# Kernel tuning notes

Measured on AMD Instinct MI355X. Metric: run time of the kernel, lower is better.

## Reference

```python
import jax, jax.numpy as jnp
import numpy as np

E = 8        # n_experts
K = 2        # top_k
D = 1024     # n_embed
H = 2048     # moe_n_hidden
B, T = 4, 2048


def setup_inputs() -> dict:
    key = jax.random.key(0)
    ks = jax.random.split(key, 6)
    s = 0.02
    return {
        "x": jax.random.normal(ks[0], (B, T, D), dtype=jnp.float32),
        "Wr": jax.random.normal(ks[1], (D, E), dtype=jnp.float32) * s,   # router weight
        "W1": jax.random.normal(ks[2], (E, D, 2 * H), dtype=jnp.float32) * s,
        "b1": jnp.zeros((E, 2 * H), dtype=jnp.float32),
        "W2": jax.random.normal(ks[3], (E, H, D), dtype=jnp.float32) * s,
        "b2": jnp.zeros((E, D), dtype=jnp.float32),
    }


def reference(x, Wr, W1, b1, W2, b2):
    b, t, d = x.shape
    # router logits (noise=0, temp=1.0)
    z = jnp.einsum('btd,de->bte', x, Wr)                 # [B,T,E]
    vals, idx = jax.lax.top_k(z, K)                      # [B,T,K]
    gates = jax.nn.softmax(vals, axis=-1)                # [B,T,K]
    # combine weights per (token, expert): sum_k gate_k * 1[idx_k == e]
    onehot = jax.nn.one_hot(idx, E, dtype=x.dtype)       # [B,T,K,E]
    comb = jnp.einsum('btk,btke->bte', gates, onehot).reshape(b * t, E)
    xf = x.reshape(b * t, d)                             # [N,D]
    out = jnp.zeros_like(xf)
    for e in range(E):  # fixed small loop over structurally-distinct experts
        ab = xf @ W1[e] + b1[e]                          # [N,2H]
        a, bb = jnp.split(ab, 2, axis=-1)
        h = jax.nn.silu(a) * bb                          # swiGLU
        y = h @ W2[e] + b2[e]                            # [N,D]
        out = out + comb[:, e:e + 1] * y
    return out.reshape(b, t, d)
```

## Files before the change

### kernel.cpp

```cpp
#include <hip/hip_runtime.h>


#define N_TOK 8192
#define DIM   1024
#define HID   2048
#define NEXP  8
#define NK    (N_TOK * 2)
#define MAXT2 72
#define MAXT1 136

typedef __attribute__((ext_vector_type(8))) short short8;
typedef __attribute__((ext_vector_type(4))) float f32x4;

#define BARX() __builtin_amdgcn_s_barrier()
#define FEN()  asm volatile("" ::: "memory")
#define VMW2() asm volatile("s_waitcnt vmcnt(2)" ::: "memory")
#define VMW1() asm volatile("s_waitcnt vmcnt(1)" ::: "memory")
#define VMW0() asm volatile("s_waitcnt vmcnt(0)" ::: "memory")
#define PRIO(p) __builtin_amdgcn_s_setprio(p)

static __device__ __forceinline__ unsigned short f2bf(float f) {
  unsigned int u = __float_as_uint(f);
  u += 0x7fffu + ((u >> 16) & 1u);
  return (unsigned short)(u >> 16);
}

static __device__ __forceinline__ void glds16(const void* g, void* l) {
  __builtin_amdgcn_global_load_lds(
      (const __attribute__((address_space(1))) unsigned int*)g,
      (__attribute__((address_space(3))) unsigned int*)l, 16, 0, 0);
}

__device__ __forceinline__ void transpose_tile(const float* __restrict__ s,
                                               unsigned short* __restrict__ d,
                                               int R, int C, int c0, int r0,
                                               unsigned short (*tT)[68]) {
  int tid = threadIdx.x;
  int c = tid & 63, rq = tid >> 6;
#pragma unroll
  for (int q = 0; q < 4; ++q) {
    int rb = q * 16 + rq * 4;
    ushort4 v;
    v.x = f2bf(s[(size_t)(r0 + rb + 0) * C + c0 + c]);
    v.y = f2bf(s[(size_t)(r0 + rb + 1) * C + c0 + c]);
    v.z = f2bf(s[(size_t)(r0 + rb + 2) * C + c0 + c]);
    v.w = f2bf(s[(size_t)(r0 + rb + 3) * C + c0 + c]);
    *(ushort4*)&tT[c][rb] = v;
  }
  __syncthreads();
#pragma unroll
  for (int it = 0; it < 4; ++it) {
    int idx = it * 256 + tid;
    int cc = idx >> 4;
    int r4 = (idx & 15) * 4;
    *(ushort4*)(d + (size_t)(c0 + cc) * R + r0 + r4) = *(const ushort4*)&tT[cc][r4];
  }
}

__global__ __launch_bounds__(256) void prep_k(
    const float* __restrict__ x, const float* __restrict__ Wr,
    const float* __restrict__ W1, const float* __restrict__ W2,
    unsigned short* __restrict__ w1t, unsigned short* __restrict__ w2t,
    unsigned short* __restrict__ xb, int* __restrict__ te,
    float* __restrict__ tg, float* __restrict__ out) {
  __shared__ unsigned short tT[64][68];
  int bid = blockIdx.x;
  if (bid < 8192) {
    int z = bid >> 10, rem = bid & 1023;
    int c0 = (rem & 63) * 64, r0 = (rem >> 6) * 64;
    transpose_tile(W1 + (size_t)z * DIM * 2 * HID,
                   w1t + (size_t)z * DIM * 2 * HID, DIM, 2 * HID, c0, r0, tT);
  } else if (bid < 12288) {
    int b2 = bid - 8192;
    int z = b2 >> 9, rem = b2 & 511;
    int c0 = (rem & 15) * 64, r0 = (rem >> 4) * 64;
    transpose_tile(W2 + (size_t)z * HID * DIM,
                   w2t + (size_t)z * HID * DIM, HID, DIM, c0, r0, tT);
  } else if (bid < 14336) {
    int n = (bid - 12288) * 4 + (threadIdx.x >> 6);
    int lane = threadIdx.x & 63;
    float z[8];
#pragma unroll
    for (int e = 0; e < 8; ++e) z[e] = 0.f;
    const float* xr = x + (size_t)n * DIM;
    unsigned short* xbr = xb + (size_t)n * DIM;
#pragma unroll 4
    for (int i = 0; i < DIM / 64; ++i) {
      int d = lane + i * 64;
      float xv = xr[d];
      xbr[d] = f2bf(xv);
      float4 w0 = *(const float4*)(Wr + (size_t)d * 8);
      float4 w1 = *(const float4*)(Wr + (size_t)d * 8 + 4);
      z[0] += xv * w0.x; z[1] += xv * w0.y; z[2] += xv * w0.z; z[3] += xv * w0.w;
      z[4] += xv * w1.x; z[5] += xv * w1.y; z[6] += xv * w1.z; z[7] += xv * w1.w;
    }
    for (int off = 32; off; off >>= 1)
#pragma unroll
      for (int e = 0; e < 8; ++e) z[e] += __shfl_down(z[e], off);
    if (lane == 0) {
      int e0 = 0; float v0 = z[0];
#pragma unroll
      for (int e = 1; e < 8; ++e) if (z[e] > v0) { v0 = z[e]; e0 = e; }
      int e1 = -1; float v1 = -3.4e38f;
#pragma unroll
      for (int e = 0; e < 8; ++e) if (e != e0 && z[e] > v1) { v1 = z[e]; e1 = e; }
      float r = expf(v1 - v0);
      float s0 = 1.f / (1.f + r);
      te[n * 2] = e0; te[n * 2 + 1] = e1;
      tg[n * 2] = s0; tg[n * 2 + 1] = r * s0;
    }
  } else {
    int t = bid - 14336;
    float4* o4 = (float4*)out;
    int idx = t * 256 + threadIdx.x;
#pragma unroll
    for (int i = 0; i < 4; ++i) o4[idx + i * 524288] = (float4){0.f, 0.f, 0.f, 0.f};
  }
}

__global__ __launch_bounds__(1024) void sortscan_k(
    const int* __restrict__ te, const float* __restrict__ tg,
    int* __restrict__ offs, int* __restrict__ tl256, int* __restrict__ tl128,
    int* __restrict__ rows, float* __restrict__ rowg) {
  __shared__ int hist[8];
  __shared__ int curs[8];
  int tid = threadIdx.x;
  if (tid < 8) hist[tid] = 0;
  __syncthreads();
  for (int i = tid; i < NK; i += 1024) atomicAdd(&hist[te[i]], 1);
  __syncthreads();
  if (tid == 0) {
    int o = 0, t2 = 0, t1 = 0;
    offs[0] = 0; tl256[0] = 0; tl128[0] = 0;
    for (int e = 0; e < NEXP; ++e) {
      curs[e] = o;
      o += hist[e];
      offs[e + 1] = o;
      t2 += (hist[e] + 255) >> 8;
      tl256[e + 1] = t2;
      t1 += (hist[e] + 127) >> 7;
      tl128[e + 1] = t1;
    }
  }
  __syncthreads();
  for (int i = tid; i < NK; i += 1024) {
    int e = te[i];
    int pos = atomicAdd(&curs[e], 1);
    rows[pos] = i >> 1;
    rowg[pos] = tg[i];
  }
}

template <int GID, int BM>
__global__ __launch_bounds__(512, 2) void moe_gemm8p(
    const unsigned short* __restrict__ Asrc,
    const unsigned short* __restrict__ Wt,
    const float* __restrict__ bias,
    unsigned short* __restrict__ hb,
    float* __restrict__ out,
    const int* __restrict__ rows,
    const float* __restrict__ rowg,
    const int* __restrict__ offs,
    const int* __restrict__ tl) {
  constexpr int KD = (GID == 0) ? DIM : HID;
  constexpr int NT = KD / 32;
  constexpr int MF = BM / 32;
  constexpr int MH = MF / 2;
  constexpr int ASZ = BM * 32;
  constexpr bool AFULL = (BM == 128);
  __shared__ unsigned short smem[2 * ASZ + 2 * 8192];

  int bt = blockIdx.x;
  if (bt >= tl[NEXP]) return;
  int e = 0;
  while (e < NEXP - 1 && bt >= tl[e + 1]) ++e;
  int rt = bt - tl[e];
  int base = offs[e];
  int cntE = offs[e + 1] - base;
  int row0 = rt * BM;
  int jb = blockIdx.y;

  int tid = threadIdx.x, lane = tid & 63, w = tid >> 6;
  int wr = w >> 2, wc = w & 3;

  int g8 = (((lane & 3) ^ ((lane >> 3) & 3)) * 8);
  const unsigned short* bP[2];
  int bD[2];
#pragma unroll
  for (int hf = 0; hf < 2; ++hf) {
    int rB = hf * 128 + w * 16 + (lane >> 2);
    if (GID == 0) {
      int j0h = jb * 128;
      int hcol = j0h + (rB >> 5) * 16 + (rB & 15);
      int w1row = hcol + ((rB >> 4) & 1) * HID;
      bP[hf] = Wt + ((size_t)e * 2 * HID + w1row) * DIM + g8;
    } else {
      int j0 = jb * 256;
      bP[hf] = Wt + ((size_t)e * DIM + (j0 + rB)) * HID + g8;
    }
    bD[hf] = (hf * 128 + w * 16) * 32;
  }
  constexpr int NAH = AFULL ? 1 : 2;
  const unsigned short* aP[NAH];
  int aD[NAH];
#pragma unroll
  for (int hf = 0; hf < NAH; ++hf) {
    int rbA;
    if (AFULL) {
      rbA = w * 16;
    } else {
      int q0 = w * 16;
      rbA = (q0 < 64 ? q0 : q0 + 64) + hf * 64;
    }
    int rA = rbA + (lane >> 2);
    int rr = row0 + rA; rr = rr < cntE ? rr : cntE - 1;
    if (GID == 0) {
      int tok = rows[base + rr];
      aP[hf] = Asrc + (size_t)tok * DIM + g8;
    } else {
      aP[hf] = Asrc + (size_t)(base + rr) * HID + g8;
    }
    aD[hf] = rbA * 32;
  }

  auto stA = [&](int t, int hf) {
    if (t < NT) glds16(aP[hf] + (size_t)t * 32, smem + (t & 1) * ASZ + aD[hf]);
  };
  auto stB = [&](int t, int hf) {
    if (t < NT) glds16(bP[hf] + (size_t)t * 32, smem + 2 * ASZ + (t & 1) * 8192 + bD[hf]);
  };

  int kg = lane >> 4;
  int koff = ((kg ^ ((lane >> 1) & 3)) * 8);
  unsigned aoff = (unsigned)((wr * (BM / 2) + (lane & 15)) * 32 + koff);
  unsigned boff = (unsigned)((wc * 64 + (lane & 15)) * 32 + koff);

  f32x4 acc[MF][4];
#pragma unroll
  for (int m = 0; m < MF; ++m)
#pragma unroll
    for (int n = 0; n < 4; ++n) acc[m][n] = (f32x4){0.f, 0.f, 0.f, 0.f};

  short8 a[MH], b[4];

#define MFMA_Q(MB, NB)                                                        \
  PRIO(1);                                                                    \
  _Pragma("unroll") for (int m = 0; m < MH; ++m)                              \
  _Pragma("unroll") for (int n = 0; n < 2; ++n)                               \
    acc[(MB) + m][(NB) + n] = __builtin_amdgcn_mfma_f32_16x16x32_bf16(        \
        a[m], b[(NB) + n], acc[(MB) + m][(NB) + n], 0, 0, 0);                 \
  PRIO(0)

  if constexpr (AFULL) {
    stA(0, 0); stB(0, 0); stB(0, 1); stA(1, 0);
    VMW1();
  } else {
    stA(0, 0); stA(0, 1); stB(0, 0); stB(0, 1); stA(1, 0); stA(1, 1);
    VMW2();
  }
  FEN(); BARX(); FEN();

  for (int it = 0; it < NT / 2; ++it) {
#pragma unroll
    for (int half = 0; half < 2; ++half) {
      int Tn = 2 * it + half;
      unsigned Ab = half ? (unsigned)ASZ : 0u;
      unsigned Bb = 2u * ASZ + (half ? 8192u : 0u);
#pragma unroll
      for (int m = 0; m < MH; ++m)
        a[m] = *(const short8*)(smem + Ab + aoff + m * 512);
#pragma unroll
      for (int n = 0; n < 2; ++n)
        b[n] = *(const short8*)(smem + Bb + boff + n * 512);
      stB(Tn + 1, 0);
      FEN(); BARX(); FEN();
      MFMA_Q(0, 0);
      FEN(); BARX(); FEN();
#pragma unroll
      for (int n = 2; n < 4; ++n)
        b[n] = *(const short8*)(smem + Bb + boff + n * 512);
      stB(Tn + 1, 1);
      FEN(); BARX(); FEN();
      MFMA_Q(0, 2);
      FEN(); BARX(); FEN();
#pragma unroll
      for (int m = 0; m < MH; ++m)
        a[m] = *(const short8*)(smem + Ab + aoff + (MH + m) * 512);
      if constexpr (!AFULL) stA(Tn + 2, 0);
      FEN(); BARX(); FEN();
      MFMA_Q(MH, 2);
      FEN(); BARX(); FEN();
      if constexpr (AFULL) stA(Tn + 2, 0); else stA(Tn + 2, 1);
      FEN(); BARX(); FEN();
      MFMA_Q(MH, 0);
      if (Tn + 2 < NT) {
        if constexpr (AFULL) { VMW1(); } else { VMW2(); }
      } else {
        VMW0();
      }
      FEN(); BARX(); FEN();
    }
  }
#undef MFMA_Q

  int rowl = lane >> 4, coll = lane & 15;
  if (GID == 0) {
    int j0h = jb * 128;
#pragma unroll
    for (int pair = 0; pair < 2; ++pair) {
      int hcol = j0h + (2 * wc + pair) * 16 + coll;
      float ba = bias[e * 2 * HID + hcol];
      float bb = bias[e * 2 * HID + HID + hcol];
#pragma unroll
      for (int m = 0; m < MF; ++m)
#pragma unroll
        for (int j = 0; j < 4; ++j) {
          int grow = row0 + wr * (BM / 2) + m * 16 + rowl * 4 + j;
          if (grow < cntE) {
            float av = acc[m][2 * pair][j] + ba;
            float bv = acc[m][2 * pair + 1][j] + bb;
            float hv = av / (1.f + __expf(-av)) * bv;
            hb[(size_t)(base + grow) * HID + hcol] = f2bf(hv);
          }
        }
    }
  } else {
    int j0 = jb * 256;
    float bv[4];
#pragma unroll
    for (int n = 0; n < 4; ++n) bv[n] = bias[e * DIM + j0 + wc * 64 + n * 16 + coll];
#pragma unroll
    for (int m = 0; m < MF; ++m)
#pragma unroll
      for (int j = 0; j < 4; ++j) {
        int grow = row0 + wr * (BM / 2) + m * 16 + rowl * 4 + j;
        if (grow < cntE) {
          int tok = rows[base + grow];
          float g = rowg[base + grow];
#pragma unroll
          for (int n = 0; n < 4; ++n) {
            int col = j0 + wc * 64 + n * 16 + coll;
            atomicAdd(&out[(size_t)tok * DIM + col], g * (acc[m][n][j] + bv[n]));
          }
        }
      }
  }
}

extern "C" void kernel_launch(void* const* d_in, const int* in_sizes, int n_in,
                              void* d_out, int out_size, void* d_ws, size_t ws_size,
                              hipStream_t stream) {
  (void)in_sizes; (void)n_in; (void)out_size;
  const float* x  = (const float*)d_in[0];
  const float* Wr = (const float*)d_in[1];
  const float* W1 = (const float*)d_in[2];
  const float* b1 = (const float*)d_in[3];
  const float* W2 = (const float*)d_in[4];
  const float* b2 = (const float*)d_in[5];
  float* out = (float*)d_out;
  char* ws = (char*)d_ws;

  const size_t o_xb   = 0;
  const size_t o_w1t  = o_xb   + (size_t)N_TOK * DIM * 2;
  const size_t o_w2t  = o_w1t  + (size_t)NEXP * 2 * HID * DIM * 2;
  const size_t o_hb   = o_w2t  + (size_t)NEXP * DIM * HID * 2;
  const size_t o_rows = o_hb   + (size_t)NK * HID * 2;
  const size_t o_rowg = o_rows + (size_t)NK * 4;
  const size_t o_te   = o_rowg + (size_t)NK * 4;
  const size_t o_tg   = o_te   + (size_t)NK * 4;
  const size_t o_offs = o_tg   + (size_t)NK * 4;
  const size_t o_t2   = o_offs + 64;
  const size_t o_t1   = o_t2   + 64;
  const size_t need   = o_t1   + 64;
  if (ws_size < need) return;

  unsigned short* xb  = (unsigned short*)(ws + o_xb);
  unsigned short* w1t = (unsigned short*)(ws + o_w1t);
  unsigned short* w2t = (unsigned short*)(ws + o_w2t);
  unsigned short* hb  = (unsigned short*)(ws + o_hb);
  int*   rows = (int*)(ws + o_rows);
  float* rowg = (float*)(ws + o_rowg);
  int*   te   = (int*)(ws + o_te);
  float* tg   = (float*)(ws + o_tg);
  int*   offs = (int*)(ws + o_offs);
  int*   tl256 = (int*)(ws + o_t2);
  int*   tl128 = (int*)(ws + o_t1);

  prep_k<<<16384, 256, 0, stream>>>(x, Wr, W1, W2, w1t, w2t, xb, te, tg, out);
  sortscan_k<<<1, 1024, 0, stream>>>(te, tg, offs, tl256, tl128, rows, rowg);
  moe_gemm8p<0, 256><<<dim3(MAXT2, HID / 128), 512, 0, stream>>>(
      xb, w1t, b1, hb, nullptr, rows, rowg, offs, tl256);
  moe_gemm8p<1, 128><<<dim3(MAXT1, DIM / 256), 512, 0, stream>>>(
      hb, w2t, b2, nullptr, out, rows, rowg, offs, tl128);
}
```

Baseline: 430.3 us.

## Replace 512-thread ping-pong GEMM with 128x128 tiled kernel and fold W2 prep into GEMM1

The hand-scheduled 8-wave ping-pong MFMA kernel (256- or 128-row tiles) is replaced with a simpler 4-wave kernel. It uses fixed 128x128 tiles, a double-buffered LDS pipeline and one barrier per k-step, with 3 blocks per CU. The W2 transpose and output zeroing move out of the prep kernel into extra blocks of the first GEMM grid, which shortens prep and overlaps that work with GEMM1. In exchange, smaller tiles mean less data reuse, and full vmcnt(0) waits each iteration reduce latency hiding.

```diff
diff --git a/kernel.cpp b/kernel.cpp
--- a/kernel.cpp
+++ b/kernel.cpp
@@ -6,16 +6,14 @@
 #define HID   2048
 #define NEXP  8
 #define NK    (N_TOK * 2)
-#define MAXT2 72
 #define MAXT1 136
+#define G1Y   272
 
 typedef __attribute__((ext_vector_type(8))) short short8;
 typedef __attribute__((ext_vector_type(4))) float f32x4;
 
 #define BARX() __builtin_amdgcn_s_barrier()
 #define FEN()  asm volatile("" ::: "memory")
-#define VMW2() asm volatile("s_waitcnt vmcnt(2)" ::: "memory")
-#define VMW1() asm volatile("s_waitcnt vmcnt(1)" ::: "memory")
 #define VMW0() asm volatile("s_waitcnt vmcnt(0)" ::: "memory")
 #define PRIO(p) __builtin_amdgcn_s_setprio(p)
 
@@ -59,10 +57,10 @@
 
 __global__ __launch_bounds__(256) void prep_k(
     const float* __restrict__ x, const float* __restrict__ Wr,
-    const float* __restrict__ W1, const float* __restrict__ W2,
-    unsigned short* __restrict__ w1t, unsigned short* __restrict__ w2t,
+    const float* __restrict__ W1,
+    unsigned short* __restrict__ w1t,
     unsigned short* __restrict__ xb, int* __restrict__ te,
-    float* __restrict__ tg, float* __restrict__ out) {
+    float* __restrict__ tg) {
   __shared__ unsigned short tT[64][68];
   int bid = blockIdx.x;
   if (bid < 8192) {
@@ -70,14 +68,8 @@
     int c0 = (rem & 63) * 64, r0 = (rem >> 6) * 64;
     transpose_tile(W1 + (size_t)z * DIM * 2 * HID,
                    w1t + (size_t)z * DIM * 2 * HID, DIM, 2 * HID, c0, r0, tT);
-  } else if (bid < 12288) {
-    int b2 = bid - 8192;
-    int z = b2 >> 9, rem = b2 & 511;
-    int c0 = (rem & 15) * 64, r0 = (rem >> 4) * 64;
-    transpose_tile(W2 + (size_t)z * HID * DIM,
-                   w2t + (size_t)z * HID * DIM, HID, DIM, c0, r0, tT);
-  } else if (bid < 14336) {
-    int n = (bid - 12288) * 4 + (threadIdx.x >> 6);
+  } else {
+    int n = (bid - 8192) * 4 + (threadIdx.x >> 6);
     int lane = threadIdx.x & 63;
     float z[8];
 #pragma unroll
@@ -109,18 +101,12 @@
       te[n * 2] = e0; te[n * 2 + 1] = e1;
       tg[n * 2] = s0; tg[n * 2 + 1] = r * s0;
     }
-  } else {
-    int t = bid - 14336;
-    float4* o4 = (float4*)out;
-    int idx = t * 256 + threadIdx.x;
-#pragma unroll
-    for (int i = 0; i < 4; ++i) o4[idx + i * 524288] = (float4){0.f, 0.f, 0.f, 0.f};
   }
 }
 
 __global__ __launch_bounds__(1024) void sortscan_k(
     const int* __restrict__ te, const float* __restrict__ tg,
-    int* __restrict__ offs, int* __restrict__ tl256, int* __restrict__ tl128,
+    int* __restrict__ offs, int* __restrict__ tl128,
     int* __restrict__ rows, float* __restrict__ rowg) {
   __shared__ int hist[8];
   __shared__ int curs[8];
@@ -130,14 +116,12 @@
   for (int i = tid; i < NK; i += 1024) atomicAdd(&hist[te[i]], 1);
   __syncthreads();
   if (tid == 0) {
-    int o = 0, t2 = 0, t1 = 0;
-    offs[0] = 0; tl256[0] = 0; tl128[0] = 0;
+    int o = 0, t1 = 0;
+    offs[0] = 0; tl128[0] = 0;
     for (int e = 0; e < NEXP; ++e) {
       curs[e] = o;
       o += hist[e];
       offs[e + 1] = o;
-      t2 += (hist[e] + 255) >> 8;
-      tl256[e + 1] = t2;
       t1 += (hist[e] + 127) >> 7;
       tl128[e + 1] = t1;
     }
@@ -151,8 +135,8 @@
   }
 }
 
-template <int GID, int BM>
-__global__ __launch_bounds__(512, 2) void moe_gemm8p(
+template <int GID>
+__global__ __launch_bounds__(256, 3) void moe_gemm2p(
     const unsigned short* __restrict__ Asrc,
     const unsigned short* __restrict__ Wt,
     const float* __restrict__ bias,
@@ -161,186 +145,155 @@
     const int* __restrict__ rows,
     const float* __restrict__ rowg,
     const int* __restrict__ offs,
-    const int* __restrict__ tl) {
+    const int* __restrict__ tl,
+    const float* __restrict__ W2f,
+    unsigned short* __restrict__ w2td,
+    float* __restrict__ outz) {
   constexpr int KD = (GID == 0) ? DIM : HID;
   constexpr int NT = KD / 32;
-  constexpr int MF = BM / 32;
-  constexpr int MH = MF / 2;
-  constexpr int ASZ = BM * 32;
-  constexpr bool AFULL = (BM == 128);
-  __shared__ unsigned short smem[2 * ASZ + 2 * 8192];
-
-  int bt = blockIdx.x;
+  __shared__ unsigned short smem[16384];
+
+  int bt = blockIdx.y;
+  if (GID == 0 && bt >= MAXT1) {
+    if (bt < MAXT1 + 128) {
+      int t = (bt - MAXT1) * 32 + (int)blockIdx.x;
+      int z = t >> 9, rem = t & 511;
+      int c0 = (rem & 15) * 64, r0 = (rem >> 4) * 64;
+      transpose_tile(W2f + (size_t)z * HID * DIM,
+                     w2td + (size_t)z * HID * DIM, HID, DIM, c0, r0,
+                     (unsigned short(*)[68])smem);
+    } else {
+      int t = (bt - MAXT1 - 128) * 32 + (int)blockIdx.x;
+      float4* o4 = (float4*)outz;
+      int idx = t * 256 + threadIdx.x;
+#pragma unroll
+      for (int i = 0; i < 32; ++i) o4[idx + i * 65536] = (float4){0.f, 0.f, 0.f, 0.f};
+    }
+    return;
+  }
   if (bt >= tl[NEXP]) return;
   int e = 0;
   while (e < NEXP - 1 && bt >= tl[e + 1]) ++e;
   int rt = bt - tl[e];
   int base = offs[e];
   int cntE = offs[e + 1] - base;
-  int row0 = rt * BM;
-  int jb = blockIdx.y;
+  int row0 = rt * 128;
+  int jb = blockIdx.x;
 
   int tid = threadIdx.x, lane = tid & 63, w = tid >> 6;
-  int wr = w >> 2, wc = w & 3;
+  int wr = w >> 1, wc = w & 1;
 
   int g8 = (((lane & 3) ^ ((lane >> 3) & 3)) * 8);
+  const unsigned short* aP[2];
   const unsigned short* bP[2];
-  int bD[2];
-#pragma unroll
-  for (int hf = 0; hf < 2; ++hf) {
-    int rB = hf * 128 + w * 16 + (lane >> 2);
-    if (GID == 0) {
-      int j0h = jb * 128;
-      int hcol = j0h + (rB >> 5) * 16 + (rB & 15);
-      int w1row = hcol + ((rB >> 4) & 1) * HID;
-      bP[hf] = Wt + ((size_t)e * 2 * HID + w1row) * DIM + g8;
-    } else {
-      int j0 = jb * 256;
-      bP[hf] = Wt + ((size_t)e * DIM + (j0 + rB)) * HID + g8;
-    }
-    bD[hf] = (hf * 128 + w * 16) * 32;
-  }
-  constexpr int NAH = AFULL ? 1 : 2;
-  const unsigned short* aP[NAH];
-  int aD[NAH];
-#pragma unroll
-  for (int hf = 0; hf < NAH; ++hf) {
-    int rbA;
-    if (AFULL) {
-      rbA = w * 16;
-    } else {
-      int q0 = w * 16;
-      rbA = (q0 < 64 ? q0 : q0 + 64) + hf * 64;
-    }
-    int rA = rbA + (lane >> 2);
+  int aD[2], bD[2];
+#pragma unroll
+  for (int s = 0; s < 2; ++s) {
+    int rA = w * 16 + (lane >> 2) + s * 64;
     int rr = row0 + rA; rr = rr < cntE ? rr : cntE - 1;
     if (GID == 0) {
       int tok = rows[base + rr];
-      aP[hf] = Asrc + (size_t)tok * DIM + g8;
+      aP[s] = Asrc + (size_t)tok * DIM + g8;
     } else {
-      aP[hf] = Asrc + (size_t)(base + rr) * HID + g8;
-    }
-    aD[hf] = rbA * 32;
-  }
-
-  auto stA = [&](int t, int hf) {
-    if (t < NT) glds16(aP[hf] + (size_t)t * 32, smem + (t & 1) * ASZ + aD[hf]);
+      aP[s] = Asrc + (size_t)(base + rr) * HID + g8;
+    }
+    aD[s] = (w * 16 + s * 64) * 32;
+    int rB = w * 16 + (lane >> 2) + s * 64;
+    if (GID == 0) {
+      int j0 = jb * 64;
+      int u = rB & 63, wcb = rB >> 6;
+      int hcol = j0 + wcb * 32 + (u & 31);
+      int w1row = hcol + (u >> 5) * HID;
+      bP[s] = Wt + ((size_t)e * 2 * HID + w1row) * DIM + g8;
+    } else {
+      bP[s] = Wt + ((size_t)e * DIM + (jb * 128 + rB)) * HID + g8;
+    }
+    bD[s] = (w * 16 + s * 64) * 32;
+  }
+
+  auto stg = [&](int t, int nxt) {
+    if (t < NT) {
+      glds16(aP[0] + (size_t)t * 32, smem + nxt * 4096 + aD[0]);
+      glds16(aP[1] + (size_t)t * 32, smem + nxt * 4096 + aD[1]);
+      glds16(bP[0] + (size_t)t * 32, smem + 8192 + nxt * 4096 + bD[0]);
+      glds16(bP[1] + (size_t)t * 32, smem + 8192 + nxt * 4096 + bD[1]);
+    }
   };
-  auto stB = [&](int t, int hf) {
-    if (t < NT) glds16(bP[hf] + (size_t)t * 32, smem + 2 * ASZ + (t & 1) * 8192 + bD[hf]);
-  };
-
-  int kg = lane >> 4;
+
+  int kg = lane >> 4, coll = lane & 15;
   int koff = ((kg ^ ((lane >> 1) & 3)) * 8);
-  unsigned aoff = (unsigned)((wr * (BM / 2) + (lane & 15)) * 32 + koff);
-  unsigned boff = (unsigned)((wc * 64 + (lane & 15)) * 32 + koff);
-
-  f32x4 acc[MF][4];
-#pragma unroll
-  for (int m = 0; m < MF; ++m)
+  unsigned aoff[4], boff[4];
+#pragma unroll
+  for (int m = 0; m < 4; ++m) aoff[m] = (unsigned)((wr * 64 + m * 16 + coll) * 32 + koff);
+#pragma unroll
+  for (int n = 0; n < 4; ++n) boff[n] = (unsigned)((wc * 64 + n * 16 + coll) * 32 + koff);
+
+  f32x4 acc[4][4];
+#pragma unroll
+  for (int m = 0; m < 4; ++m)
 #pragma unroll
     for (int n = 0; n < 4; ++n) acc[m][n] = (f32x4){0.f, 0.f, 0.f, 0.f};
 
-  short8 a[MH], b[4];
-
-#define MFMA_Q(MB, NB)                                                        \
-  PRIO(1);                                                                    \
-  _Pragma("unroll") for (int m = 0; m < MH; ++m)                              \
-  _Pragma("unroll") for (int n = 0; n < 2; ++n)                               \
-    acc[(MB) + m][(NB) + n] = __builtin_amdgcn_mfma_f32_16x16x32_bf16(        \
-        a[m], b[(NB) + n], acc[(MB) + m][(NB) + n], 0, 0, 0);                 \
-  PRIO(0)
-
-  if constexpr (AFULL) {
-    stA(0, 0); stB(0, 0); stB(0, 1); stA(1, 0);
-    VMW1();
-  } else {
-    stA(0, 0); stA(0, 1); stB(0, 0); stB(0, 1); stA(1, 0); stA(1, 1);
-    VMW2();
-  }
-  FEN(); BARX(); FEN();
-
-  for (int it = 0; it < NT / 2; ++it) {
-#pragma unroll
-    for (int half = 0; half < 2; ++half) {
-      int Tn = 2 * it + half;
-      unsigned Ab = half ? (unsigned)ASZ : 0u;
-      unsigned Bb = 2u * ASZ + (half ? 8192u : 0u);
-#pragma unroll
-      for (int m = 0; m < MH; ++m)
-        a[m] = *(const short8*)(smem + Ab + aoff + m * 512);
-#pragma unroll
-      for (int n = 0; n < 2; ++n)
-        b[n] = *(const short8*)(smem + Bb + boff + n * 512);
-      stB(Tn + 1, 0);
-      FEN(); BARX(); FEN();
-      MFMA_Q(0, 0);
-      FEN(); BARX(); FEN();
-#pragma unroll
-      for (int n = 2; n < 4; ++n)
-        b[n] = *(const short8*)(smem + Bb + boff + n * 512);
-      stB(Tn + 1, 1);
-      FEN(); BARX(); FEN();
-      MFMA_Q(0, 2);
-      FEN(); BARX(); FEN();
-#pragma unroll
-      for (int m = 0; m < MH; ++m)
-        a[m] = *(const short8*)(smem + Ab + aoff + (MH + m) * 512);
-      if constexpr (!AFULL) stA(Tn + 2, 0);
-      FEN(); BARX(); FEN();
-      MFMA_Q(MH, 2);
-      FEN(); BARX(); FEN();
-      if constexpr (AFULL) stA(Tn + 2, 0); else stA(Tn + 2, 1);
-      FEN(); BARX(); FEN();
-      MFMA_Q(MH, 0);
-      if (Tn + 2 < NT) {
-        if constexpr (AFULL) { VMW1(); } else { VMW2(); }
-      } else {
-        VMW0();
-      }
-      FEN(); BARX(); FEN();
-    }
-  }
-#undef MFMA_Q
-
-  int rowl = lane >> 4, coll = lane & 15;
+  short8 a[4], b[4];
+
+  stg(0, 0);
+  VMW0(); FEN(); BARX(); FEN();
+
+  int cur = 0;
+  for (int t = 0; t < NT; ++t) {
+    stg(t + 1, cur ^ 1);
+#pragma unroll
+    for (int m = 0; m < 4; ++m)
+      a[m] = *(const short8*)(smem + cur * 4096 + aoff[m]);
+#pragma unroll
+    for (int n = 0; n < 4; ++n)
+      b[n] = *(const short8*)(smem + 8192 + cur * 4096 + boff[n]);
+    PRIO(1);
+#pragma unroll
+    for (int m = 0; m < 4; ++m)
+#pragma unroll
+      for (int n = 0; n < 4; ++n)
+        acc[m][n] = __builtin_amdgcn_mfma_f32_16x16x32_bf16(a[m], b[n], acc[m][n], 0, 0, 0);
+    PRIO(0);
+    VMW0(); FEN(); BARX(); FEN();
+    cur ^= 1;
+  }
+
+  int rowl = lane >> 4;
   if (GID == 0) {
-    int j0h = jb * 128;
-#pragma unroll
-    for (int pair = 0; pair < 2; ++pair) {
-      int hcol = j0h + (2 * wc + pair) * 16 + coll;
+    int j0 = jb * 64;
+#pragma unroll
+    for (int n = 0; n < 2; ++n) {
+      int hcol = j0 + wc * 32 + n * 16 + coll;
       float ba = bias[e * 2 * HID + hcol];
       float bb = bias[e * 2 * HID + HID + hcol];
 #pragma unroll
-      for (int m = 0; m < MF; ++m)
+      for (int m = 0; m < 4; ++m)
 #pragma unroll
         for (int j = 0; j < 4; ++j) {
-          int grow = row0 + wr * (BM / 2) + m * 16 + rowl * 4 + j;
+          int grow = row0 + wr * 64 + m * 16 + rowl * 4 + j;
           if (grow < cntE) {
-            float av = acc[m][2 * pair][j] + ba;
-            float bv = acc[m][2 * pair + 1][j] + bb;
+            float av = acc[m][n][j] + ba;
+            float bv = acc[m][n + 2][j] + bb;
             float hv = av / (1.f + __expf(-av)) * bv;
             hb[(size_t)(base + grow) * HID + hcol] = f2bf(hv);
           }
         }
     }
   } else {
-    int j0 = jb * 256;
-    float bv[4];
-#pragma unroll
-    for (int n = 0; n < 4; ++n) bv[n] = bias[e * DIM + j0 + wc * 64 + n * 16 + coll];
-#pragma unroll
-    for (int m = 0; m < MF; ++m)
+#pragma unroll
+    for (int m = 0; m < 4; ++m)
 #pragma unroll
       for (int j = 0; j < 4; ++j) {
-        int grow = row0 + wr * (BM / 2) + m * 16 + rowl * 4 + j;
+        int grow = row0 + wr * 64 + m * 16 + rowl * 4 + j;
         if (grow < cntE) {
           int tok = rows[base + grow];
           float g = rowg[base + grow];
 #pragma unroll
           for (int n = 0; n < 4; ++n) {
-            int col = j0 + wc * 64 + n * 16 + coll;
-            atomicAdd(&out[(size_t)tok * DIM + col], g * (acc[m][n][j] + bv[n]));
+            int col = jb * 128 + wc * 64 + n * 16 + coll;
+            atomicAdd(&out[(size_t)tok * DIM + col],
+                      g * (acc[m][n][j] + bias[e * DIM + col]));
           }
         }
       }
@@ -369,8 +322,7 @@
   const size_t o_te   = o_rowg + (size_t)NK * 4;
   const size_t o_tg   = o_te   + (size_t)NK * 4;
   const size_t o_offs = o_tg   + (size_t)NK * 4;
-  const size_t o_t2   = o_offs + 64;
-  const size_t o_t1   = o_t2   + 64;
+  const size_t o_t1   = o_offs + 64;
   const size_t need   = o_t1   + 64;
   if (ws_size < need) return;
 
@@ -383,13 +335,12 @@
   int*   te   = (int*)(ws + o_te);
   float* tg   = (float*)(ws + o_tg);
   int*   offs = (int*)(ws + o_offs);
-  int*   tl256 = (int*)(ws + o_t2);
   int*   tl128 = (int*)(ws + o_t1);
 
-  prep_k<<<16384, 256, 0, stream>>>(x, Wr, W1, W2, w1t, w2t, xb, te, tg, out);
-  sortscan_k<<<1, 1024, 0, stream>>>(te, tg, offs, tl256, tl128, rows, rowg);
-  moe_gemm8p<0, 256><<<dim3(MAXT2, HID / 128), 512, 0, stream>>>(
-      xb, w1t, b1, hb, nullptr, rows, rowg, offs, tl256);
-  moe_gemm8p<1, 128><<<dim3(MAXT1, DIM / 256), 512, 0, stream>>>(
-      hb, w2t, b2, nullptr, out, rows, rowg, offs, tl128);
-}
+  prep_k<<<10240, 256, 0, stream>>>(x, Wr, W1, w1t, xb, te, tg);
+  sortscan_k<<<1, 1024, 0, stream>>>(te, tg, offs, tl128, rows, rowg);
+  moe_gemm2p<0><<<dim3(HID / 64, G1Y), 256, 0, stream>>>(
+      xb, w1t, b1, hb, nullptr, rows, rowg, offs, tl128, W2, w2t, out);
+  moe_gemm2p<1><<<dim3(DIM / 128, MAXT1), 256, 0, stream>>>(
+      hb, w2t, b2, nullptr, out, rows, rowg, offs, tl128, nullptr, nullptr, nullptr);
+}
```

Result: faster. 418.6 us (-2.7%).
